# Kernel tuning notes

Hardware: AMD Instinct MI355X
Metric: run time of the kernel (lower is better)

## Reference

```python
import jax, jax.numpy as jnp
import numpy as np

K1, K2 = 2, 4  # kernels of the two channel groups
BN_EPS = 1e-5


def _neocell_group(x, wa, wb, k):
    # Block-diagonal (a @ x) @ b with a k x k block repeated along the diagonal
    # per channel (NeoCellRepeat): equivalent to blockwise transforms on H and W.
    B, c, H, W = x.shape
    xb = x.reshape(B, c, H // k, k, W // k, k)
    y = jnp.einsum('cpi,bcnimj,cjq->bcnpmq', wa, xb, wb)
    return y.reshape(B, c, H, W)


def setup_inputs() -> dict:
    key = jax.random.key(0)
    ks = jax.random.split(key, 12)
    B, C, H, W = 32, 256, 56, 56
    c1, c2 = 128, 128
    Ci = 4 * C  # inner_mult = 4
    x = jax.random.normal(ks[0], (B, C, H, W), dtype=jnp.float32)
    wa1 = jax.random.normal(ks[1], (c1, K1, K1), dtype=jnp.float32) / np.float32(np.sqrt(K1))
    wb1 = jax.random.normal(ks[2], (c1, K1, K1), dtype=jnp.float32) / np.float32(np.sqrt(K1))
    wa2 = jax.random.normal(ks[3], (c2, K2, K2), dtype=jnp.float32) / np.float32(np.sqrt(K2))
    wb2 = jax.random.normal(ks[4], (c2, K2, K2), dtype=jnp.float32) / np.float32(np.sqrt(K2))
    bn_weight = 1.0 + 0.1 * jax.random.normal(ks[5], (C,), dtype=jnp.float32)
    bn_bias = 0.1 * jax.random.normal(ks[6], (C,), dtype=jnp.float32)
    bn_mean = 0.1 * jax.random.normal(ks[7], (C,), dtype=jnp.float32)
    bn_var = jax.random.uniform(ks[8], (C,), dtype=jnp.float32, minval=0.5, maxval=1.5)
    fc1_w = jax.random.normal(ks[9], (Ci, C), dtype=jnp.float32) / np.float32(np.sqrt(C))
    fc2_w = jax.random.normal(ks[10], (C, Ci), dtype=jnp.float32) / np.float32(np.sqrt(Ci))
    return {"x": x, "wa1": wa1, "wb1": wb1, "wa2": wa2, "wb2": wb2,
            "bn_weight": bn_weight, "bn_bias": bn_bias, "bn_mean": bn_mean,
            "bn_var": bn_var, "fc1_w": fc1_w, "fc2_w": fc2_w}


def reference(x, wa1, wb1, wa2, wb2, bn_weight, bn_bias, bn_mean, bn_var, fc1_w, fc2_w):
    c1 = wa1.shape[0]
    # NeoCell: per-group block-diagonal (a @ x) @ b
    y = jnp.concatenate([
        _neocell_group(x[:, :c1], wa1, wb1, K1),
        _neocell_group(x[:, c1:], wa2, wb2, K2),
    ], axis=1)
    # BatchNorm2d (eval mode, running stats)
    inv = jax.lax.rsqrt(bn_var + BN_EPS)
    scale = (bn_weight * inv)[None, :, None, None]
    shift = (bn_bias - bn_mean * bn_weight * inv)[None, :, None, None]
    y = y * scale + shift
    # chw -> hwc, MLP with exact GELU, hwc -> chw
    y = jnp.transpose(y, (0, 2, 3, 1))
    h = jax.nn.gelu(y @ fc1_w.T, approximate=False)
    y = h @ fc2_w.T
    y = jnp.transpose(y, (0, 3, 1, 2))
    # residual (drop_path = 0)
    return y + x
```

## Files before the change

kernel.cpp:

```cpp
#include <hip/hip_runtime.h>
#include <stdint.h>

typedef __bf16 bf16x8 __attribute__((ext_vector_type(8)));
typedef float f32x4 __attribute__((ext_vector_type(4)));

__device__ __forceinline__ float bf2f(uint16_t u) {
  union { uint32_t i; float f; } v; v.i = ((uint32_t)u) << 16; return v.f;
}
__device__ __forceinline__ uint16_t f2bf(float f) {
  union { float f; uint32_t i; } v; v.f = f;
  uint32_t u = v.i;
  uint32_t r = (u + 0x7FFFu + ((u >> 16) & 1u)) >> 16;
  return (uint16_t)r;
}
__device__ __forceinline__ float fast_gelu(float v) {
  float t2 = v * v;
  float pz = 1.0f + 0.044715f * t2;
  float w = -1.5957691216f * v * pz;
  float e = __expf(w);
  return v * __builtin_amdgcn_rcpf(1.0f + e);
}
__device__ __forceinline__ void gld16(uint16_t* l, const uint16_t* g) {
  __builtin_amdgcn_global_load_lds(
      (const __attribute__((address_space(1))) void*)g,
      (__attribute__((address_space(3))) void*)l, 16, 0, 0);
}

__global__ __launch_bounds__(256) void cvt_weights_kernel(
    const float* __restrict__ fc1, const float* __restrict__ fc2,
    uint16_t* __restrict__ fc1b, uint16_t* __restrict__ fc2b)
{
  int i = (blockIdx.x * 256 + threadIdx.x) * 4;
  if (i < 262144) {
    float4 a = *(const float4*)(fc1 + i);
    ushort4 o;
    o.x = f2bf(a.x); o.y = f2bf(a.y); o.z = f2bf(a.z); o.w = f2bf(a.w);
    *(ushort4*)(fc1b + i) = o;
  } else {
    int j = i - 262144;
    float4 a = *(const float4*)(fc2 + j);
    ushort4 o;
    o.x = f2bf(a.x); o.y = f2bf(a.y); o.z = f2bf(a.z); o.w = f2bf(a.w);
    *(ushort4*)(fc2b + j) = o;
  }
}

__global__ __launch_bounds__(128) void neocell_bn_kernel(
    const float* __restrict__ x,
    const float* __restrict__ wa1, const float* __restrict__ wb1,
    const float* __restrict__ wa2, const float* __restrict__ wb2,
    const float* __restrict__ bnw, const float* __restrict__ bnb,
    const float* __restrict__ bnm, const float* __restrict__ bnv,
    uint16_t* __restrict__ y1)
{
  __shared__ uint16_t lx[64 * 226];
  const int t = threadIdx.x;
  const int strip = blockIdx.x;
  const int b = blockIdx.y;
  const int grp = blockIdx.z;
  const int h0 = strip * 4;

  for (int i = 0; i < 28; ++i) {
    int l = t + i * 128;
    int c = l / 56;
    int r = l - c * 56;
    const float* g = x + (size_t)(b * 256 + grp * 64 + c) * 3136
                       + h0 * 56 + r * 4;
    float4 v = *(const float4*)g;
    ushort4 o;
    o.x = f2bf(v.x); o.y = f2bf(v.y); o.z = f2bf(v.z); o.w = f2bf(v.w);
    *(ushort4*)(lx + c * 226 + r * 4) = o;
  }
  __syncthreads();

  const int c = t & 63;
  const int p = t >> 6;
  const int cg = grp * 64 + c;

  const float sc = bnw[cg] * rsqrtf(bnv[cg] + 1e-5f);
  const float sh = bnb[cg] - bnm[cg] * sc;
  const size_t pgbase = (size_t)b * 3136 + (size_t)h0 * 56;
  const uint16_t* lc0 = lx + c * 226;

  if (grp < 2) {
    float A[2][2], Bm[2][2];
#pragma unroll
    for (int i = 0; i < 2; ++i)
#pragma unroll
      for (int j = 0; j < 2; ++j) {
        A[i][j]  = wa1[cg * 4 + i * 2 + j];
        Bm[i][j] = wb1[cg * 4 + i * 2 + j];
      }
    for (int m = 0; m < 28; ++m) {
      const uint16_t* lc = lc0 + (2 * p) * 56 + m * 2;
      uint32_t w0 = *(const uint32_t*)lc;
      uint32_t w1 = *(const uint32_t*)(lc + 56);
      float X[2][2];
      X[0][0] = bf2f((uint16_t)w0); X[0][1] = bf2f((uint16_t)(w0 >> 16));
      X[1][0] = bf2f((uint16_t)w1); X[1][1] = bf2f((uint16_t)(w1 >> 16));
      float T[2][2];
#pragma unroll
      for (int pp = 0; pp < 2; ++pp)
#pragma unroll
        for (int j = 0; j < 2; ++j)
          T[pp][j] = A[pp][0] * X[0][j] + A[pp][1] * X[1][j];
#pragma unroll
      for (int pp = 0; pp < 2; ++pp)
#pragma unroll
        for (int q = 0; q < 2; ++q) {
          float O = (T[pp][0] * Bm[0][q] + T[pp][1] * Bm[1][q]) * sc + sh;
          size_t pg = pgbase + (size_t)(2 * p + pp) * 56 + (m * 2 + q);
          y1[pg * 256 + cg] = f2bf(O);
        }
    }
  } else {
    const int ck = cg - 128;
    float A[4][4], Bm[4][4];
#pragma unroll
    for (int i = 0; i < 4; ++i)
#pragma unroll
      for (int j = 0; j < 4; ++j) {
        A[i][j]  = wa2[ck * 16 + i * 4 + j];
        Bm[i][j] = wb2[ck * 16 + i * 4 + j];
      }
    for (int mm = 0; mm < 7; ++mm) {
      int m = 2 * mm + p;
      float X[4][4];
#pragma unroll
      for (int i = 0; i < 4; ++i) {
        const uint16_t* lc = lc0 + i * 56 + m * 4;
        uint32_t w0 = *(const uint32_t*)lc;
        uint32_t w1 = *(const uint32_t*)(lc + 2);
        X[i][0] = bf2f((uint16_t)w0); X[i][1] = bf2f((uint16_t)(w0 >> 16));
        X[i][2] = bf2f((uint16_t)w1); X[i][3] = bf2f((uint16_t)(w1 >> 16));
      }
      float T[4][4];
#pragma unroll
      for (int pp = 0; pp < 4; ++pp)
#pragma unroll
        for (int j = 0; j < 4; ++j)
          T[pp][j] = A[pp][0] * X[0][j] + A[pp][1] * X[1][j]
                   + A[pp][2] * X[2][j] + A[pp][3] * X[3][j];
#pragma unroll
      for (int pp = 0; pp < 4; ++pp)
#pragma unroll
        for (int q = 0; q < 4; ++q) {
          float O = (T[pp][0] * Bm[0][q] + T[pp][1] * Bm[1][q]
                   + T[pp][2] * Bm[2][q] + T[pp][3] * Bm[3][q]) * sc + sh;
          size_t pg = pgbase + (size_t)pp * 56 + (m * 4 + q);
          y1[pg * 256 + cg] = f2bf(O);
        }
    }
  }
}

template <int KD, int EPI>
__global__ __launch_bounds__(256) void gemm_bt_kernel(
    const uint16_t* __restrict__ A,
    const uint16_t* __restrict__ Bw,
    uint16_t* __restrict__ Cb16,
    float* __restrict__ Cf32,
    const float* __restrict__ Xres,
    int chunk_pix0)
{
  __shared__ uint16_t lds[16640];
  uint16_t* A0 = lds;
  uint16_t* B0 = lds + 4096;
  uint16_t* A1 = lds + 8192;
  uint16_t* B1 = lds + 12288;

  const int tid = threadIdx.x;
  const int lane = tid & 63;
  const int wid = tid >> 6;
  const int wm = wid & 1;
  const int wn = wid >> 1;
  const int fm = lane & 15;
  const int fq = lane >> 4;

  uint32_t nx = gridDim.x;
  uint32_t n = nx * gridDim.y;
  uint32_t lid = blockIdx.y * nx + blockIdx.x;
  uint32_t bx, by;
  if ((n & 7u) == 0u) {
    uint32_t w = (lid & 7u) * (n >> 3) + (lid >> 3);
    bx = w & (nx - 1u);
    by = w / nx;
  } else {
    bx = blockIdx.x; by = blockIdx.y;
  }

  const size_t arow0 = (size_t)by * 128;
  const size_t brow0 = (size_t)bx * 128;

  f32x4 acc[4][4];
#pragma unroll
  for (int i = 0; i < 4; ++i)
#pragma unroll
    for (int j = 0; j < 4; ++j) { f32x4 z = {0.f, 0.f, 0.f, 0.f}; acc[i][j] = z; }

  const int q0 = tid, q1 = tid + 256;
  const int r0 = q0 >> 2, kk0 = q0 & 3;
  const int r1 = q1 >> 2, kk1 = q1 & 3;
  const uint16_t* a0 = A + (arow0 + r0) * KD + kk0 * 8;
  const uint16_t* a1 = A + (arow0 + r1) * KD + kk1 * 8;
  const uint16_t* b0 = Bw + (brow0 + r0) * KD + kk0 * 8;
  const uint16_t* b1 = Bw + (brow0 + r1) * KD + kk1 * 8;

  auto phase = [&](const uint16_t* cA, const uint16_t* cB,
                   uint16_t* nA, uint16_t* nB, int kn) {
    gld16(nA + q0 * 8, a0 + kn);
    gld16(nA + q1 * 8, a1 + kn);
    gld16(nB + q0 * 8, b0 + kn);
    gld16(nB + q1 * 8, b1 + kn);
    bf16x8 af[4], bfr[4];
#pragma unroll
    for (int mt = 0; mt < 4; ++mt)
      af[mt] = *(const bf16x8*)(const void*)
               (cA + (wm * 64 + mt * 16 + fm) * 32 + fq * 8);
#pragma unroll
    for (int nt = 0; nt < 4; ++nt)
      bfr[nt] = *(const bf16x8*)(const void*)
                (cB + (wn * 64 + nt * 16 + fm) * 32 + fq * 8);
#pragma unroll
    for (int mt = 0; mt < 4; ++mt)
#pragma unroll
      for (int nt = 0; nt < 4; ++nt)
        acc[mt][nt] = __builtin_amdgcn_mfma_f32_16x16x32_bf16(
            af[mt], bfr[nt], acc[mt][nt], 0, 0, 0);
    __syncthreads();
  };

  gld16(A0 + q0 * 8, a0);
  gld16(A0 + q1 * 8, a1);
  gld16(B0 + q0 * 8, b0);
  gld16(B0 + q1 * 8, b1);
  __syncthreads();

  constexpr int NT = KD / 32;
#pragma unroll 1
  for (int t = 0; t < NT; t += 2) {
    phase(A0, B0, A1, B1, ((t + 1) & (NT - 1)) * 32);
    phase(A1, B1, A0, B0, ((t + 2) & (NT - 1)) * 32);
  }

  if (EPI == 0) {
#pragma unroll
    for (int mt = 0; mt < 4; ++mt) {
      const size_t rb = arow0 + wm * 64 + mt * 16 + fq * 4;
#pragma unroll
      for (int nt = 0; nt < 4; ++nt) {
        const size_t n2 = brow0 + wn * 64 + nt * 16 + fm;
#pragma unroll
        for (int r = 0; r < 4; ++r)
          Cb16[(rb + r) * 1024 + n2] = f2bf(fast_gelu(acc[mt][nt][r]));
      }
    }
  } else {
    __syncthreads();
#pragma unroll
    for (int mt = 0; mt < 4; ++mt) {
      int mbase = wm * 64 + mt * 16 + fq * 4;
#pragma unroll
      for (int nt = 0; nt < 4; ++nt) {
        int nn = wn * 64 + nt * 16 + fm;
#pragma unroll
        for (int r = 0; r < 4; ++r)
          lds[nn * 130 + mbase + r] = f2bf(acc[mt][nt][r]);
      }
    }
    __syncthreads();
    const int pl0 = tid & 31;
    const int cw = tid >> 5;
#pragma unroll
    for (int it = 0; it < 16; ++it) {
      int ch = cw + it * 8;
      int cgl = (int)brow0 + ch;
#pragma unroll
      for (int e = 0; e < 4; ++e) {
        int pl = pl0 + e * 32;
        uint32_t pg = (uint32_t)chunk_pix0 + by * 128u + (uint32_t)pl;
        uint32_t bimg = pg / 3136u;
        uint32_t rem = pg - bimg * 3136u;
        size_t addr = ((size_t)bimg * 256 + cgl) * 3136 + rem;
        Cf32[addr] = bf2f(lds[ch * 130 + pl]) + Xres[addr];
      }
    }
  }
}

extern "C" void kernel_launch(void* const* d_in, const int* in_sizes, int n_in,
                              void* d_out, int out_size, void* d_ws,
                              size_t ws_size, hipStream_t stream)
{
  const float* x   = (const float*)d_in[0];
  const float* wa1 = (const float*)d_in[1];
  const float* wb1 = (const float*)d_in[2];
  const float* wa2 = (const float*)d_in[3];
  const float* wb2 = (const float*)d_in[4];
  const float* bnw = (const float*)d_in[5];
  const float* bnb = (const float*)d_in[6];
  const float* bnm = (const float*)d_in[7];
  const float* bnv = (const float*)d_in[8];
  const float* fc1 = (const float*)d_in[9];
  const float* fc2 = (const float*)d_in[10];
  float* out = (float*)d_out;

  uint16_t* fc1b = (uint16_t*)d_ws;
  uint16_t* fc2b = fc1b + 262144;
  uint16_t* y1 = fc2b + 262144;
  const size_t y1_elems = (size_t)100352 * 256;
  uint16_t* h = y1 + y1_elems;

  const long tiles_total = 784;
  const size_t fixed_bytes = (size_t)262144 * 4 + y1_elems * 2;
  long tiles_chunk = 1;
  if (ws_size > fixed_bytes + 262144) {
    tiles_chunk = (long)((ws_size - fixed_bytes) / (128ul * 1024ul * 2ul));
    if (tiles_chunk > tiles_total) tiles_chunk = tiles_total;
    if (tiles_chunk < 1) tiles_chunk = 1;
  }

  cvt_weights_kernel<<<512, 256, 0, stream>>>(fc1, fc2, fc1b, fc2b);
  neocell_bn_kernel<<<dim3(14, 32, 4), 128, 0, stream>>>(
      x, wa1, wb1, wa2, wb2, bnw, bnb, bnm, bnv, y1);

  for (long t0 = 0; t0 < tiles_total; t0 += tiles_chunk) {
    long T = tiles_total - t0;
    if (T > tiles_chunk) T = tiles_chunk;
    gemm_bt_kernel<256, 0><<<dim3(8, (uint32_t)T), 256, 0, stream>>>(
        y1 + (size_t)t0 * 128 * 256, fc1b, h, nullptr, nullptr, 0);
    gemm_bt_kernel<1024, 1><<<dim3(2, (uint32_t)T), 256, 0, stream>>>(
        h, fc2b, nullptr, out, x, (int)(t0 * 128));
  }
}
```

Measured before the change: 412.3 us.

## Switch GEMM main loop to triple-buffered LDS with two tiles in flight

After: 433.2 us. 1.05x slower.

```diff
diff --git a/kernel.cpp b/kernel.cpp
--- a/kernel.cpp
+++ b/kernel.cpp
@@ -163,11 +163,7 @@
     const float* __restrict__ Xres,
     int chunk_pix0)
 {
-  __shared__ uint16_t lds[16640];
-  uint16_t* A0 = lds;
-  uint16_t* B0 = lds + 4096;
-  uint16_t* A1 = lds + 8192;
-  uint16_t* B1 = lds + 12288;
+  __shared__ uint16_t lds[24576];
 
   const int tid = threadIdx.x;
   const int lane = tid & 63;
@@ -206,41 +202,52 @@
   const uint16_t* b0 = Bw + (brow0 + r0) * KD + kk0 * 8;
   const uint16_t* b1 = Bw + (brow0 + r1) * KD + kk1 * 8;
 
-  auto phase = [&](const uint16_t* cA, const uint16_t* cB,
-                   uint16_t* nA, uint16_t* nB, int kn) {
-    gld16(nA + q0 * 8, a0 + kn);
-    gld16(nA + q1 * 8, a1 + kn);
-    gld16(nB + q0 * 8, b0 + kn);
-    gld16(nB + q1 * 8, b1 + kn);
+  constexpr int NT = KD / 32;
+
+  auto stage = [&](uint16_t* S, int kt) {
+    const int ke = kt * 32;
+    gld16(S + q0 * 8, a0 + ke);
+    gld16(S + q1 * 8, a1 + ke);
+    gld16(S + 4096 + q0 * 8, b0 + ke);
+    gld16(S + 4096 + q1 * 8, b1 + ke);
+  };
+
+  stage(lds, 0);
+  stage(lds + 8192, 1);
+
+  int cur = 0, nxt = 2;
+#pragma unroll 1
+  for (int t = 0; t < NT; ++t) {
+    int kn = t + 2; if (kn > NT - 1) kn = NT - 1;
+    stage(lds + nxt * 8192, kn);
+    asm volatile("s_waitcnt vmcnt(8)" ::: "memory");
+    __builtin_amdgcn_s_barrier();
+    asm volatile("" ::: "memory");
+
+    const uint16_t* CA = lds + cur * 8192;
+    const uint16_t* CB = CA + 4096;
     bf16x8 af[4], bfr[4];
 #pragma unroll
     for (int mt = 0; mt < 4; ++mt)
       af[mt] = *(const bf16x8*)(const void*)
-               (cA + (wm * 64 + mt * 16 + fm) * 32 + fq * 8);
+               (CA + (wm * 64 + mt * 16 + fm) * 32 + fq * 8);
 #pragma unroll
     for (int nt = 0; nt < 4; ++nt)
       bfr[nt] = *(const bf16x8*)(const void*)
-                (cB + (wn * 64 + nt * 16 + fm) * 32 + fq * 8);
+                (CB + (wn * 64 + nt * 16 + fm) * 32 + fq * 8);
 #pragma unroll
     for (int mt = 0; mt < 4; ++mt)
 #pragma unroll
       for (int nt = 0; nt < 4; ++nt)
         acc[mt][nt] = __builtin_amdgcn_mfma_f32_16x16x32_bf16(
             af[mt], bfr[nt], acc[mt][nt], 0, 0, 0);
-    __syncthreads();
-  };
-
-  gld16(A0 + q0 * 8, a0);
-  gld16(A0 + q1 * 8, a1);
-  gld16(B0 + q0 * 8, b0);
-  gld16(B0 + q1 * 8, b1);
-  __syncthreads();
-
-  constexpr int NT = KD / 32;
-#pragma unroll 1
-  for (int t = 0; t < NT; t += 2) {
-    phase(A0, B0, A1, B1, ((t + 1) & (NT - 1)) * 32);
-    phase(A1, B1, A0, B0, ((t + 2) & (NT - 1)) * 32);
+
+    asm volatile("" ::: "memory");
+    __builtin_amdgcn_s_barrier();
+    asm volatile("" ::: "memory");
+
+    cur = (cur == 2) ? 0 : cur + 1;
+    nxt = (nxt == 2) ? 0 : nxt + 1;
   }
 
   if (EPI == 0) {
```

## Double K-tile depth to 64 with XOR-swizzled LDS layout in GEMM kernel

Applied to the files above, without the earlier changes.

After: 419.9 us. About the same (+1.8%).

```diff
diff --git a/kernel.cpp b/kernel.cpp
--- a/kernel.cpp
+++ b/kernel.cpp
@@ -163,11 +163,11 @@
     const float* __restrict__ Xres,
     int chunk_pix0)
 {
-  __shared__ uint16_t lds[16640];
+  __shared__ uint16_t lds[32768];
   uint16_t* A0 = lds;
-  uint16_t* B0 = lds + 4096;
-  uint16_t* A1 = lds + 8192;
-  uint16_t* B1 = lds + 12288;
+  uint16_t* B0 = lds + 8192;
+  uint16_t* A1 = lds + 16384;
+  uint16_t* B1 = lds + 24576;
 
   const int tid = threadIdx.x;
   const int lane = tid & 63;
@@ -198,49 +198,59 @@
 #pragma unroll
     for (int j = 0; j < 4; ++j) { f32x4 z = {0.f, 0.f, 0.f, 0.f}; acc[i][j] = z; }
 
-  const int q0 = tid, q1 = tid + 256;
-  const int r0 = q0 >> 2, kk0 = q0 & 3;
-  const int r1 = q1 >> 2, kk1 = q1 & 3;
-  const uint16_t* a0 = A + (arow0 + r0) * KD + kk0 * 8;
-  const uint16_t* a1 = A + (arow0 + r1) * KD + kk1 * 8;
-  const uint16_t* b0 = Bw + (brow0 + r0) * KD + kk0 * 8;
-  const uint16_t* b1 = Bw + (brow0 + r1) * KD + kk1 * 8;
-
-  auto phase = [&](const uint16_t* cA, const uint16_t* cB,
-                   uint16_t* nA, uint16_t* nB, int kn) {
-    gld16(nA + q0 * 8, a0 + kn);
-    gld16(nA + q1 * 8, a1 + kn);
-    gld16(nB + q0 * 8, b0 + kn);
-    gld16(nB + q1 * 8, b1 + kn);
-    bf16x8 af[4], bfr[4];
-#pragma unroll
-    for (int mt = 0; mt < 4; ++mt)
-      af[mt] = *(const bf16x8*)(const void*)
-               (cA + (wm * 64 + mt * 16 + fm) * 32 + fq * 8);
-#pragma unroll
-    for (int nt = 0; nt < 4; ++nt)
-      bfr[nt] = *(const bf16x8*)(const void*)
-                (cB + (wn * 64 + nt * 16 + fm) * 32 + fq * 8);
-#pragma unroll
-    for (int mt = 0; mt < 4; ++mt)
-#pragma unroll
-      for (int nt = 0; nt < 4; ++nt)
-        acc[mt][nt] = __builtin_amdgcn_mfma_f32_16x16x32_bf16(
-            af[mt], bfr[nt], acc[mt][nt], 0, 0, 0);
-    __syncthreads();
+  auto stage = [&](uint16_t* SA, uint16_t* SB, int kt) {
+    const int ke = kt * 64;
+#pragma unroll
+    for (int s = 0; s < 4; ++s) {
+      int q = tid + s * 256;
+      int r = q >> 3;
+      int kkg = (q & 7) ^ (r & 7);
+      gld16(SA + q * 8, A + (arow0 + r) * KD + ke + kkg * 8);
+      gld16(SB + q * 8, Bw + (brow0 + r) * KD + ke + kkg * 8);
+    }
   };
 
-  gld16(A0 + q0 * 8, a0);
-  gld16(A0 + q1 * 8, a1);
-  gld16(B0 + q0 * 8, b0);
-  gld16(B0 + q1 * 8, b1);
+  const int sxA = fq ^ (fm & 7);
+
+  auto compute = [&](const uint16_t* CA, const uint16_t* CB) {
+#pragma unroll
+    for (int h = 0; h < 2; ++h) {
+      bf16x8 af[4], bfr[4];
+#pragma unroll
+      for (int mt = 0; mt < 4; ++mt) {
+        int row = wm * 64 + mt * 16 + fm;
+        int sl = (h * 4 + fq) ^ (fm & 7);
+        af[mt] = *(const bf16x8*)(const void*)(CA + row * 64 + sl * 8);
+      }
+#pragma unroll
+      for (int nt = 0; nt < 4; ++nt) {
+        int row = wn * 64 + nt * 16 + fm;
+        int sl = (h * 4 + fq) ^ (fm & 7);
+        bfr[nt] = *(const bf16x8*)(const void*)(CB + row * 64 + sl * 8);
+      }
+#pragma unroll
+      for (int mt = 0; mt < 4; ++mt)
+#pragma unroll
+        for (int nt = 0; nt < 4; ++nt)
+          acc[mt][nt] = __builtin_amdgcn_mfma_f32_16x16x32_bf16(
+              af[mt], bfr[nt], acc[mt][nt], 0, 0, 0);
+    }
+  };
+  (void)sxA;
+
+  constexpr int NT = KD / 64;
+
+  stage(A0, B0, 0);
   __syncthreads();
 
-  constexpr int NT = KD / 32;
 #pragma unroll 1
   for (int t = 0; t < NT; t += 2) {
-    phase(A0, B0, A1, B1, ((t + 1) & (NT - 1)) * 32);
-    phase(A1, B1, A0, B0, ((t + 2) & (NT - 1)) * 32);
+    stage(A1, B1, (t + 1) & (NT - 1));
+    compute(A0, B0);
+    __syncthreads();
+    stage(A0, B0, (t + 2) & (NT - 1));
+    compute(A1, B1);
+    __syncthreads();
   }
 
   if (EPI == 0) {
```
